# Optimization experiments

Hardware: AMD Instinct MI355X
Metric: run time of the kernel (lower is better)

Reference implementation:

```python
import jax, jax.numpy as jnp
import numpy as np
from jax import lax

B, C, L = 4, 256, 4
NA, NS, NAR = 3, 5, 4          # anchors, states, arrows
PRED_C = 4 + 1 + NS + NAR + 1  # 15 channels per anchor
HW = [(192, 320), (96, 160), (48, 80), (24, 40)]
EPS = 1e-5


def conv2d(x, w, b, pad):
    # x: (B,Cin,H,W), w: (Cout,Cin,kh,kw)
    y = lax.conv_general_dilated(x, w, (1, 1), ((pad, pad), (pad, pad)),
                                 dimension_numbers=('NCHW', 'OIHW', 'NCHW'))
    return y + b[None, :, None, None]


def bn(x, g, beta, m, v):
    # BatchNorm2d in inference mode with running stats
    scale = (g / jnp.sqrt(v + EPS))[None, :, None, None]
    return (x - m[None, :, None, None]) * scale + beta[None, :, None, None]


def setup_inputs() -> dict:
    key = jax.random.key(0)
    d = {}
    for i, (h, w) in enumerate(HW):
        d[f"feat{i}"] = jax.random.normal(jax.random.fold_in(key, i), (B, C, h, w), jnp.float32)
    ks = jax.random.split(jax.random.fold_in(key, 100), 8)
    d["adapt_w"] = jax.random.normal(ks[0], (L, C, C, 1, 1), jnp.float32) * 0.02
    d["adapt_b"] = jnp.zeros((L, C), jnp.float32)
    d["w1"] = jax.random.normal(ks[1], (L, C, C, 3, 3), jnp.float32) * 0.02
    d["b1"] = jnp.zeros((L, C), jnp.float32)
    d["g1"] = jnp.ones((L, C), jnp.float32)
    d["be1"] = jnp.zeros((L, C), jnp.float32)
    d["m1"] = jnp.zeros((L, C), jnp.float32)
    d["v1"] = jnp.ones((L, C), jnp.float32)
    d["w2"] = jax.random.normal(ks[2], (L, C, C, 3, 3), jnp.float32) * 0.02
    d["b2"] = jnp.zeros((L, C), jnp.float32)
    d["g2"] = jnp.ones((L, C), jnp.float32)
    d["be2"] = jnp.zeros((L, C), jnp.float32)
    d["m2"] = jnp.zeros((L, C), jnp.float32)
    d["v2"] = jnp.ones((L, C), jnp.float32)
    d["wp"] = jax.random.normal(ks[3], (L, NA * PRED_C, C, 1, 1), jnp.float32) * 0.02
    d["bp"] = jnp.zeros((L, NA * PRED_C), jnp.float32)
    return d


def reference(feat0, feat1, feat2, feat3, adapt_w, adapt_b,
              w1, b1, g1, be1, m1, v1,
              w2, b2, g2, be2, m2, v2, wp, bp):
    feats = [feat0, feat1, feat2, feat3]
    outs = []
    for i in range(L):
        x = conv2d(feats[i], adapt_w[i], adapt_b[i], 0)           # fpn_adapt 1x1
        x = jax.nn.relu(bn(conv2d(x, w1[i], b1[i], 1), g1[i], be1[i], m1[i], v1[i]))
        x = jax.nn.relu(bn(conv2d(x, w2[i], b2[i], 1), g2[i], be2[i], m2[i], v2[i]))
        p = conv2d(x, wp[i], bp[i], 0)                             # (B,45,H,W)
        Bb, _, H, W = p.shape
        p = p.reshape(Bb, NA, PRED_C, H, W)
        bbox = p[:, :, 0:4]
        obj = jax.nn.sigmoid(p[:, :, 4:5])
        state = p[:, :, 5:5 + NS]
        arrow = p[:, :, 5 + NS:5 + NS + NAR]
        dist = jax.nn.softplus(p[:, :, -1:]) + 1.0
        outs += [bbox, obj, state, arrow, dist]
    return tuple(outs)
```

## Files before the change

kernel.cpp:

```cpp
#include <hip/hip_runtime.h>
#include <math.h>

typedef __attribute__((ext_vector_type(8))) short bf16x8;
typedef __attribute__((ext_vector_type(4))) float f32x4;
typedef __attribute__((ext_vector_type(4))) unsigned short us4;

#define EPSV 1e-5f

__device__ inline unsigned short f2bf(float f){
  unsigned u = __float_as_uint(f);
  u += 0x7fff + ((u>>16)&1);
  return (unsigned short)(u>>16);
}

__device__ __forceinline__ void gload16(const unsigned short* g, char* l){
  __builtin_amdgcn_global_load_lds(
      (const __attribute__((address_space(1))) unsigned int*)g,
      (__attribute__((address_space(3))) unsigned int*)l, 16, 0, 0);
}

__global__ __launch_bounds__(256) void k_trans(const float* __restrict__ feat,
    unsigned short* __restrict__ ft, int H, int W, int Wp, int y_begin,
    int slot_base, int RBf)
{
  int t = threadIdx.x;
  int lane = t & 63, wv = t >> 6;
  int x = blockIdx.x*64 + lane;
  int y = y_begin + blockIdx.y;
  int b = blockIdx.z;
  int slot = slot_base + blockIdx.y;
  if (x >= W) return;
  const float* fb = feat + ((size_t)(b*256)*H + y)*W + x;
  unsigned short* dst = ft + (((size_t)b*RBf + slot)*Wp + x + 1)*256;
  #pragma unroll 4
  for (int i=0;i<16;i++){
    int c0 = wv*4 + i*16;
    float v0 = fb[(size_t)(c0+0)*H*W];
    float v1 = fb[(size_t)(c0+1)*H*W];
    float v2 = fb[(size_t)(c0+2)*H*W];
    float v3 = fb[(size_t)(c0+3)*H*W];
    us4 o = { f2bf(v0), f2bf(v1), f2bf(v2), f2bf(v3) };
    *(us4*)(dst + c0) = o;
  }
}

__global__ __launch_bounds__(256) void k_zrow(unsigned short* __restrict__ buf,
    long bStr, int Wp, int slot0, int nslots)
{
  long i = ((long)blockIdx.x*256 + threadIdx.x)*8;
  long per_b = (long)nslots*Wp*256;
  if (i >= 4*per_b) return;
  int b = (int)(i / per_b); long r = i % per_b;
  unsigned short* d = buf + (size_t)b*bStr + (size_t)slot0*Wp*256 + r;
  us4 z = {0,0,0,0};
  *(us4*)d = z; *(us4*)(d+4) = z;
}

__global__ __launch_bounds__(256) void k_zcol(unsigned short* __restrict__ buf,
    int Wp, int RB, int W)
{
  long i = ((long)blockIdx.x*256 + threadIdx.x)*8;
  long tot = (long)4*RB*2*256;
  if (i >= tot) return;
  long u = i/8; int q = (int)(u & 31); int side = (int)((u>>5)&1);
  long bs = u>>6; int slot = (int)(bs % RB); int b = (int)(bs / RB);
  unsigned short* d = buf + (((size_t)b*RB + slot)*Wp + (side? W+1 : 0))*256 + q*8;
  us4 z = {0,0,0,0};
  *(us4*)d = z; *(us4*)(d+4) = z;
}

__global__ __launch_bounds__(256) void k_repack_conv(const float* __restrict__ w,
    const float* __restrict__ g, const float* __restrict__ v,
    unsigned short* __restrict__ wf)
{
  int t = blockIdx.x*256 + threadIdx.x;
  if (t >= 4*256*256) return;
  int ci = t & 255, co = (t>>8) & 255, l = t>>16;
  float s = g[l*256+co] * rsqrtf(v[l*256+co] + EPSV);
  const float* wp = w + (size_t)t*9;
  int cb = co>>4, kc = ci>>5;
  int lane = ((ci>>3)&3)*16 + (co&15);
  int e = ci&7;
  size_t base = (((size_t)(l*16+cb)*8 + kc)*9)*512 + (size_t)lane*8 + e;
  #pragma unroll
  for (int tap=0;tap<9;tap++)
    wf[base + (size_t)tap*512] = f2bf(wp[tap]*s);
}

__global__ __launch_bounds__(256) void k_repack_conv_raw(const float* __restrict__ w,
    unsigned short* __restrict__ wf)
{
  int t = blockIdx.x*256 + threadIdx.x;
  if (t >= 4*256*256) return;
  int ci = t & 255, co = (t>>8) & 255, l = t>>16;
  const float* wp = w + (size_t)t*9;
  int cb = co>>4, kc = ci>>5;
  int lane = ((ci>>3)&3)*16 + (co&15);
  int e = ci&7;
  size_t base = (((size_t)(l*16+cb)*8 + kc)*9)*512 + (size_t)lane*8 + e;
  #pragma unroll
  for (int tap=0;tap<9;tap++)
    wf[base + (size_t)tap*512] = f2bf(wp[tap]);
}

__global__ __launch_bounds__(256) void k_repack_awB(const float* __restrict__ aw,
    unsigned short* __restrict__ out)
{
  int t = blockIdx.x*256 + threadIdx.x;
  if (t >= 4*16*8*64) return;
  int lane = t & 63, kc = (t>>6)&7, cit = (t>>9)&15, l = t>>13;
  int ci = cit*16 + (lane&15);
  int m0 = kc*32 + ((lane>>4))*8;
  unsigned short tmp[8];
  #pragma unroll
  for (int e=0;e<8;e++)
    tmp[e] = f2bf(aw[ ((size_t)(l*256 + m0 + e))*256 + ci ]);
  unsigned short* d = out + (size_t)t*8;
  *(us4*)d = *(us4*)tmp; *(us4*)(d+4) = *(us4*)(tmp+4);
}

__global__ __launch_bounds__(256) void k_fold(
    const unsigned short* __restrict__ w1raw,
    const unsigned short* __restrict__ bawB,
    const float* __restrict__ g, const float* __restrict__ v,
    unsigned short* __restrict__ wf)
{
  int blk = blockIdx.x;
  int cich = blk & 3;
  int tap  = (blk>>2) % 9;
  int l    = blk / 36;
  int tid = threadIdx.x, lane = tid&63, w = tid>>6;
  int l15 = lane&15, g4 = lane>>4;
  f32x4 acc[4][4];
  #pragma unroll
  for (int i=0;i<4;i++)
    #pragma unroll
    for (int j=0;j<4;j++) acc[i][j] = (f32x4){0.f,0.f,0.f,0.f};

  #pragma unroll 1
  for (int kc=0; kc<8; ++kc){
    bf16x8 A[4], B[4];
    #pragma unroll
    for (int cf=0;cf<4;cf++)
      A[cf] = *(const bf16x8*)(w1raw +
        ((((size_t)(l*16 + w*4+cf)*8 + kc)*9 + tap)*512) + (size_t)lane*8);
    #pragma unroll
    for (int pf=0;pf<4;pf++)
      B[pf] = *(const bf16x8*)(bawB +
        (((size_t)(l*16 + cich*4+pf)*8 + kc)*512) + (size_t)lane*8);
    #pragma unroll
    for (int cf=0;cf<4;cf++)
      #pragma unroll
      for (int pf=0;pf<4;pf++)
        acc[cf][pf] = __builtin_amdgcn_mfma_f32_16x16x32_bf16(A[cf], B[pf], acc[cf][pf], 0,0,0);
  }
  #pragma unroll
  for (int cf=0;cf<4;cf++){
    #pragma unroll
    for (int pf=0;pf<4;pf++){
      int ci = cich*64 + pf*16 + l15;
      #pragma unroll
      for (int r=0;r<4;r++){
        int co = w*64 + cf*16 + g4*4 + r;
        float s = g[l*256+co] * rsqrtf(v[l*256+co] + EPSV);
        float val = acc[cf][pf][r] * s;
        int cb = co>>4, kci = ci>>5;
        int dlane = ((ci>>3)&3)*16 + (co&15);
        int e = ci&7;
        wf[ ((((size_t)(l*16+cb)*8 + kci)*9 + tap)*512) + (size_t)dlane*8 + e ] = f2bf(val);
      }
    }
  }
}

__global__ __launch_bounds__(192) void k_repack_pred(const float* __restrict__ w,
    unsigned short* __restrict__ wf)
{
  int t = blockIdx.x*192 + threadIdx.x;
  if (t >= 4*48*32) return;
  int o = t & 31, co = (t>>5)%48, l = t/1536;
  int ci0 = o*8, f = co>>4, kc = o>>2, lane = (o&3)*16 + (co&15);
  unsigned short* dst = wf + ((((size_t)l*8 + kc)*3 + f)*64 + lane)*8;
  #pragma unroll
  for (int e=0;e<8;e++){
    float val = (co<45) ? w[((size_t)(l*45+co)*256 + ci0 + e)] : 0.f;
    dst[e] = f2bf(val);
  }
}

__global__ __launch_bounds__(256) void k_bias(const float* __restrict__ b,
    const float* __restrict__ g, const float* __restrict__ be,
    const float* __restrict__ m, const float* __restrict__ v,
    float* __restrict__ out)
{
  int t = blockIdx.x*256 + threadIdx.x;
  if (t >= 1024) return;
  float s = g[t]*rsqrtf(v[t]+EPSV);
  out[t] = (b[t]-m[t])*s + be[t];
}

__global__ __launch_bounds__(256) void k_bias1f(
    const float* __restrict__ w1, const float* __restrict__ ab,
    const float* __restrict__ b1, const float* __restrict__ g1,
    const float* __restrict__ be1, const float* __restrict__ m1,
    const float* __restrict__ v1, float* __restrict__ bcase)
{
  int t = blockIdx.x*256 + threadIdx.x;
  if (t >= 1024) return;
  int co = t & 255, l = t >> 8;
  float tt[9] = {0,0,0,0,0,0,0,0,0};
  const float* wp  = w1 + ((size_t)(l*256+co)*256)*9;
  const float* abp = ab + l*256;
  for (int m=0;m<256;m++){
    float a = abp[m];
    const float* w9 = wp + (size_t)m*9;
    #pragma unroll
    for (int tap=0;tap<9;tap++) tt[tap] += w9[tap]*a;
  }
  float s = g1[t]*rsqrtf(v1[t]+EPSV);
  float base = be1[t] + s*(b1[t]-m1[t]);
  for (int yc=0;yc<3;yc++)
    for (int xc=0;xc<3;xc++){
      float sum = 0.f;
      #pragma unroll
      for (int tap=0;tap<9;tap++){
        int ky = tap/3, kx = tap%3;
        bool oob = (yc==0&&ky==0)||(yc==2&&ky==2)||(xc==0&&kx==0)||(xc==2&&kx==2);
        if (!oob) sum += tt[tap];
      }
      bcase[ ((size_t)(l*9) + yc*3+xc)*256 + co ] = base + s*sum;
    }
}

template<int TAPS, bool RELU, bool PRED, bool FOLD>
__global__ __launch_bounds__(256,2) void k_conv6(
    const unsigned short* __restrict__ in, const unsigned short* __restrict__ wf,
    const float* __restrict__ bias, unsigned short* __restrict__ outb,
    int W, int Wp, int y_begin, int y_end, int in_row0, int RBin,
    int out_row0, int RBout,
    const unsigned short* __restrict__ wfP, const float* __restrict__ bp,
    float* __restrict__ outP, int H)
{
  constexpr bool T9    = (TAPS==9);
  constexpr int ROWS   = T9 ? 4 : 2;
  constexpr int PXS    = T9 ? 72 : 64;
  constexpr int RSTR   = PXS*64;
  constexpr int BUFB   = ROWS*RSTR;
  constexpr int NCHK   = BUFB/1024;
  constexpr int NFULL  = NCHK/4;
  constexpr int NTAIL  = NCHK - NFULL*4;
  constexpr int CPW    = NFULL + (NTAIL?1:0);
  constexpr int PERROW = PXS*4;
  constexpr int LDSB   = PRED ? (2*BUFB > 65536 ? 2*BUFB : 65536) : 2*BUFB;
  __shared__ __align__(1024) char lds[LDSB];

  int tid = threadIdx.x, lane = tid&63, w = tid>>6;
  int l15 = lane&15, g4 = lane>>4;
  int x0 = blockIdx.x*64;
  int y0 = y_begin + 2*blockIdx.y;
  int b  = blockIdx.z;

  size_t rowEl = (size_t)Wp*256;
  const unsigned short* gb =
      in + ((size_t)b*RBin + (y0-1-in_row0))*rowEl + (size_t)x0*256;

  int Poff[CPW], Coff[CPW];
  #pragma unroll
  for (int i=0;i<CPW;i++){
    int c = (i<NFULL) ? (4*i + w) : (4*NFULL + w);
    int s = c*64 + lane;
    int r = s / PERROW;
    int rem = s - r*PERROW;
    int px = rem>>2, sq = rem&3;
    int slot = sq ^ (px&3) ^ ((px>>2)&3);
    Poff[i] = r*(int)rowEl + px*256 + slot*8;
    Coff[i] = c*1024;
  }

  int vb[12];
  #pragma unroll
  for (int kx=0;kx<3;kx++)
    #pragma unroll
    for (int pf=0;pf<4;pf++){
      int px = pf*16 + l15 + kx;
      vb[kx*4+pf] = px*64 + ((g4 ^ (px&3) ^ ((px>>2)&3))<<4);
    }

  const unsigned short* wA = wf + (size_t)(w*4)*(8*TAPS*512) + (size_t)lane*8;

  f32x4 acc0[4][4], acc1[4][4];
  #pragma unroll
  for (int i=0;i<4;i++)
    #pragma unroll
    for (int j=0;j<4;j++){
      acc0[i][j] = (f32x4){0.f,0.f,0.f,0.f};
      acc1[i][j] = (f32x4){0.f,0.f,0.f,0.f};
    }

  const unsigned short* gbk = gb;
  auto stage = [&](int jb){
    #pragma unroll
    for (int i=0;i<NFULL;i++) gload16(gbk + Poff[i], (char*)&lds[0] + jb + Coff[i]);
    if constexpr (NTAIL > 0){
      if (w < NTAIL) gload16(gbk + Poff[NFULL], (char*)&lds[0] + jb + Coff[NFULL]);
    }
    gbk += 32;
  };

#define LOADB(KY, KX, BV) { \
  _Pragma("unroll") \
  for (int pf=0;pf<4;pf++) BV[pf] = *(const bf16x8*)(base + (KY)*RSTR + vb[(KX)*4+pf]); }

#define LOADA(G, AV) { \
  _Pragma("unroll") \
  for (int cf=0;cf<4;cf++) AV[cf] = *(const bf16x8*)(wk + (size_t)cf*(8*TAPS*512) + (G)*512); }

#define MM(AC, AV, BV) { \
  _Pragma("unroll") for (int cf=0;cf<4;cf++) \
  _Pragma("unroll") for (int pf=0;pf<4;pf++) \
    AC[cf][pf] = __builtin_amdgcn_mfma_f32_16x16x32_bf16(AV[cf], BV[pf], AC[cf][pf], 0,0,0); }

  auto compute = [&](int kc, const char* base){
    const unsigned short* wk = wA + (size_t)kc*(TAPS*512);
    bf16x8 A[4], B0[4], B1[4];
    #pragma unroll
    for (int kx=0;kx<3;kx++){
      LOADB(0,kx,B0) LOADB(1,kx,B1)
      LOADA(0*3+kx,A) MM(acc0,A,B0) MM(acc1,A,B1)
      LOADB(2,kx,B0)
      LOADA(1*3+kx,A) MM(acc0,A,B1) MM(acc1,A,B0)
      LOADB(3,kx,B1)
      LOADA(2*3+kx,A) MM(acc0,A,B0) MM(acc1,A,B1)
    }
  };

  stage(0);
  __syncthreads();
  #pragma unroll 1
  for (int kt=0; kt<4; ++kt){
    stage(BUFB);
    compute(2*kt, (const char*)&lds[0]);
    __syncthreads();
    if (kt < 3) stage(0);
    compute(2*kt+1, (const char*)&lds[0] + BUFB);
    __syncthreads();
  }
#undef LOADB
#undef LOADA
#undef MM

  if constexpr (!PRED){
    bool ok1 = (y0 + 1) < y_end;
    int oslot = y0 - out_row0;
    unsigned short* ob = outb + ((size_t)b*RBout + oslot)*rowEl + 256;
    int yc0 = 1, yc1 = 1;
    if constexpr (FOLD){
      yc0 = (y0==0)?0:((y0==H-1)?2:1);
      yc1 = (y0+1==0)?0:((y0+1==H-1)?2:1);
    }
    #pragma unroll
    for (int cf=0; cf<4; ++cf){
      int co0 = w*64 + cf*16 + g4*4;
      f32x4 bbI = *(const f32x4*)(bias + (FOLD ? 4*256 : 0) + co0);
      #pragma unroll
      for (int pf=0; pf<4; ++pf){
        int x = x0 + pf*16 + l15;
        if (x < W){
          f32x4 b0 = bbI, b1v = bbI;
          if constexpr (FOLD){
            int xc = (x==0)?0:((x==W-1)?2:1);
            b0  = *(const f32x4*)(bias + (yc0*3+xc)*256 + co0);
            b1v = *(const f32x4*)(bias + (yc1*3+xc)*256 + co0);
          }
          float v0 = acc0[cf][pf][0]+b0[0], v1 = acc0[cf][pf][1]+b0[1];
          float v2 = acc0[cf][pf][2]+b0[2], v3 = acc0[cf][pf][3]+b0[3];
          if (RELU){ v0=fmaxf(v0,0.f); v1=fmaxf(v1,0.f); v2=fmaxf(v2,0.f); v3=fmaxf(v3,0.f); }
          us4 o = { f2bf(v0), f2bf(v1), f2bf(v2), f2bf(v3) };
          *(us4*)(ob + (size_t)x*256 + co0) = o;
          if (ok1){
            float u0 = acc1[cf][pf][0]+b1v[0], u1 = acc1[cf][pf][1]+b1v[1];
            float u2 = acc1[cf][pf][2]+b1v[2], u3 = acc1[cf][pf][3]+b1v[3];
            if (RELU){ u0=fmaxf(u0,0.f); u1=fmaxf(u1,0.f); u2=fmaxf(u2,0.f); u3=fmaxf(u3,0.f); }
            us4 o1 = { f2bf(u0), f2bf(u1), f2bf(u2), f2bf(u3) };
            *(us4*)(ob + rowEl + (size_t)x*256 + co0) = o1;
          }
        }
      }
    }
  } else {
    __syncthreads();
    unsigned short* xs = (unsigned short*)&lds[0];
    #pragma unroll
    for (int cf=0; cf<4; ++cf){
      int co0 = w*64 + cf*16 + g4*4;
      f32x4 bb = *(const f32x4*)(bias + co0);
      int c16 = co0 >> 3;
      int sub = (g4 & 1) * 8;
      #pragma unroll
      for (int pf=0; pf<4; ++pf){
        int px = pf*16 + l15;
        int slot = c16 ^ (px & 31);
        float v0 = fmaxf(acc0[cf][pf][0]+bb[0],0.f), v1 = fmaxf(acc0[cf][pf][1]+bb[1],0.f);
        float v2 = fmaxf(acc0[cf][pf][2]+bb[2],0.f), v3 = fmaxf(acc0[cf][pf][3]+bb[3],0.f);
        us4 o0 = { f2bf(v0), f2bf(v1), f2bf(v2), f2bf(v3) };
        *(us4*)((char*)xs + ((px*32 + slot)<<4) + sub) = o0;
        float u0 = fmaxf(acc1[cf][pf][0]+bb[0],0.f), u1 = fmaxf(acc1[cf][pf][1]+bb[1],0.f);
        float u2 = fmaxf(acc1[cf][pf][2]+bb[2],0.f), u3 = fmaxf(acc1[cf][pf][3]+bb[3],0.f);
        us4 o1 = { f2bf(u0), f2bf(u1), f2bf(u2), f2bf(u3) };
        *(us4*)((char*)xs + 32768 + ((px*32 + slot)<<4) + sub) = o1;
      }
    }
    __syncthreads();

    int rw2 = w & 1, pxg = w >> 1;
    f32x4 ap[3][2];
    #pragma unroll
    for (int f=0;f<3;f++){ ap[f][0] = (f32x4){0,0,0,0}; ap[f][1] = (f32x4){0,0,0,0}; }
    #pragma unroll
    for (int kc=0;kc<8;kc++){
      bf16x8 Bf[2];
      #pragma unroll
      for (int t2=0;t2<2;t2++){
        int px = (pxg*2+t2)*16 + l15;
        int slot = (kc*4 + g4) ^ (px & 31);
        Bf[t2] = *(const bf16x8*)((char*)xs + rw2*32768 + ((px*32 + slot)<<4));
      }
      #pragma unroll
      for (int f=0;f<3;f++){
        bf16x8 Af = *(const bf16x8*)(wfP + (((size_t)kc*3 + f)*64 + lane)*8);
        ap[f][0] = __builtin_amdgcn_mfma_f32_16x16x32_bf16(Af, Bf[0], ap[f][0], 0,0,0);
        ap[f][1] = __builtin_amdgcn_mfma_f32_16x16x32_bf16(Af, Bf[1], ap[f][1], 0,0,0);
      }
    }
    int y = y0 + rw2;
    if (y < y_end){
      size_t S = (size_t)H*W;
      #pragma unroll
      for (int f=0;f<3;f++){
        #pragma unroll
        for (int t2=0;t2<2;t2++){
          int px = x0 + (pxg*2+t2)*16 + l15;
          if (px < W){
            #pragma unroll
            for (int r=0;r<4;r++){
              int co = f*16 + g4*4 + r;
              if (co < 45){
                float val = ap[f][t2][r] + bp[co];
                int a_idx = co/15, c = co%15;
                int cum,c0,n;
                if (c<4)       {cum=0;c0=0;n=4;}
                else if (c==4) {cum=4;c0=4;n=1;}
                else if (c<10) {cum=5;c0=5;n=5;}
                else if (c<14) {cum=10;c0=10;n=4;}
                else           {cum=14;c0=14;n=1;}
                if (c==4) val = 1.f/(1.f+expf(-val));
                else if (c==14) val = (val>20.f? val : log1pf(expf(val))) + 1.f;
                size_t chan = ((size_t)(12*cum) + (size_t)((b*3+a_idx)*n + (c-c0)))*S;
                outP[chan + (size_t)y*W + px] = val;
              }
            }
          }
        }
      }
    }
  }
}

extern "C" void kernel_launch(void* const* d_in, const int* in_sizes, int n_in,
                              void* d_out, int out_size, void* d_ws, size_t ws_size,
                              hipStream_t stream)
{
  static const int Hs[4] = {192,96,48,24};
  static const int Wd[4] = {320,160,80,40};
  const float* feat[4] = {(const float*)d_in[0],(const float*)d_in[1],
                          (const float*)d_in[2],(const float*)d_in[3]};
  const float* adapt_w = (const float*)d_in[4];
  const float* adapt_b = (const float*)d_in[5];
  const float* w1 = (const float*)d_in[6];  const float* b1 = (const float*)d_in[7];
  const float* g1 = (const float*)d_in[8];  const float* be1= (const float*)d_in[9];
  const float* m1 = (const float*)d_in[10]; const float* v1 = (const float*)d_in[11];
  const float* w2 = (const float*)d_in[12]; const float* b2 = (const float*)d_in[13];
  const float* g2 = (const float*)d_in[14]; const float* be2= (const float*)d_in[15];
  const float* m2 = (const float*)d_in[16]; const float* v2 = (const float*)d_in[17];
  const float* wp = (const float*)d_in[18]; const float* bp = (const float*)d_in[19];
  float* out = (float*)d_out;

  char* base = (char*)d_ws;
  size_t off = 0;
  auto alloc = [&](size_t bytes)->char*{
    char* p = base + off; off = (off + bytes + 255) & ~(size_t)255; return p; };

  const size_t WF3_L = (size_t)16*8*9*512;
  const size_t WAB_L = (size_t)16*8*512;
  const size_t WFP_L = (size_t)8*3*512;
  unsigned short* wf1raw = (unsigned short*)alloc(4*WF3_L*2);
  unsigned short* bawB   = (unsigned short*)alloc(4*WAB_L*2);
  unsigned short* wf1f   = (unsigned short*)alloc(4*WF3_L*2);
  unsigned short* wf2    = (unsigned short*)alloc(4*WF3_L*2);
  unsigned short* wfP    = (unsigned short*)alloc(4*WFP_L*2);
  float* bcase1 = (float*)alloc(4*9*256*4);
  float* biasc2 = (float*)alloc(1024*4);
  char*  bufbase = base + off;
  size_t rem = (ws_size > off + 65536) ? (ws_size - off - 65536) : 0;

  k_repack_conv_raw<<<dim3(1024), dim3(256), 0, stream>>>(w1, wf1raw);
  k_repack_awB     <<<dim3(128),  dim3(256), 0, stream>>>(adapt_w, bawB);
  k_repack_conv    <<<dim3(1024), dim3(256), 0, stream>>>(w2, g2, v2, wf2);
  k_repack_pred    <<<dim3(32),   dim3(192), 0, stream>>>(wp, wfP);
  k_bias1f<<<dim3(4), dim3(256), 0, stream>>>(w1, adapt_b, b1, g1, be1, m1, v1, bcase1);
  k_bias  <<<dim3(4), dim3(256), 0, stream>>>(b2, g2, be2, m2, v2, biasc2);
  k_fold  <<<dim3(144), dim3(256), 0, stream>>>(wf1raw, bawB, g1, v1, wf1f);

  size_t out_off = 0;
  for (int l=0;l<4;l++){
    int H = Hs[l], W = Wd[l], Wp = W + 2;
    size_t S = (size_t)H*W;
    size_t rowEl = (size_t)Wp*256;
    long slotsAvail = (long)(rem / (rowEl*2));
    long Rl = (slotsAvail - 60) / 8;
    int R = (int)(Rl < 2 ? 2 : (Rl > H ? (long)H : Rl));
    int RBf = R + 4, RB1 = R + 2;
    unsigned short* featT = (unsigned short*)bufbase;
    unsigned short* buf1  = featT + ((size_t)4*RBf + 8)*rowEl;
    int nPxT = (W + 63) / 64;
    long zcGrid0 = ((long)4*RBf*2*256 + 2047)/2048;
    long zcGrid1 = ((long)4*RB1*2*256 + 2047)/2048;
    k_zcol<<<dim3((unsigned)zcGrid0), dim3(256), 0, stream>>>(featT, Wp, RBf, W);
    k_zcol<<<dim3((unsigned)zcGrid1), dim3(256), 0, stream>>>(buf1, Wp, RB1, W);

    for (int r0 = 0; r0 < H; r0 += R){
      int r1 = (r0 + R < H) ? (r0 + R) : H;
      int Rc = r1 - r0;
      int ya0 = (r0-2 < 0) ? 0 : r0-2;
      int ya1 = (r1+2 > H) ? H : r1+2;
      int yb0 = (r0-1 < 0) ? 0 : r0-1;
      int yb1 = (r1+1 > H) ? H : r1+1;

      if (r0 == 0){
        long zg = ((long)4*2*Wp*256 + 2047)/2048;
        k_zrow<<<dim3((unsigned)zg), dim3(256), 0, stream>>>(featT, (long)RBf*Wp*256, Wp, 0, 2);
        long zg1 = ((long)4*1*Wp*256 + 2047)/2048;
        k_zrow<<<dim3((unsigned)zg1), dim3(256), 0, stream>>>(buf1, (long)RB1*Wp*256, Wp, 0, 1);
      }
      if (r1 == H){
        long zg = ((long)4*2*Wp*256 + 2047)/2048;
        k_zrow<<<dim3((unsigned)zg), dim3(256), 0, stream>>>(featT, (long)RBf*Wp*256, Wp, Rc+2, 2);
        long zg1 = ((long)4*1*Wp*256 + 2047)/2048;
        k_zrow<<<dim3((unsigned)zg1), dim3(256), 0, stream>>>(buf1, (long)RB1*Wp*256, Wp, Rc+1, 1);
      }

      k_trans<<<dim3(nPxT, ya1-ya0, 4), dim3(256), 0, stream>>>(
          feat[l], featT, H, W, Wp, ya0, ya0-(r0-2), RBf);

      k_conv6<9,true,false,true><<<dim3(nPxT, (yb1-yb0+1)/2, 4), dim3(256), 0, stream>>>(
          featT, wf1f + (size_t)l*WF3_L, bcase1 + (size_t)l*9*256, buf1,
          W, Wp, yb0, yb1, r0-2, RBf, r0-1, RB1,
          nullptr, nullptr, nullptr, H);

      k_conv6<9,true,true,false><<<dim3(nPxT, (Rc+1)/2, 4), dim3(256), 0, stream>>>(
          buf1, wf2 + (size_t)l*WF3_L, biasc2 + l*256, nullptr,
          W, Wp, r0, r1, r0-1, RB1, 0, 0,
          wfP + (size_t)l*WFP_L, bp + l*45, out + out_off, H);
    }
    out_off += (size_t)4*45*S;
  }
}
```

Measured before the change: 1.538 ms.

## Batch all pyramid levels into single fused transpose and conv launches

Adds a fused path used when the workspace can hold every level's full padded buffers at once. Halo zeroing, the feature transpose, conv1 and conv2+prediction each run as one launch across all four levels, with a per-block level lookup through cumulative block counts. This removes the per-level, per-row-chunk launch loop and the tail underfill of small levels. The cost is a larger workspace footprint and some extra index arithmetic per block.

```diff
diff --git a/kernel.cpp b/kernel.cpp
--- a/kernel.cpp
+++ b/kernel.cpp
@@ -17,6 +17,303 @@
   __builtin_amdgcn_global_load_lds(
       (const __attribute__((address_space(1))) unsigned int*)g,
       (__attribute__((address_space(3))) unsigned int*)l, 16, 0, 0);
+}
+
+struct TrP {
+  int cum[5];
+  int W[4], Wp[4], H[4], nPx[4];
+  unsigned long long ftOff[4];
+};
+struct CvP {
+  int cum[5];
+  int W[4], Wp[4], H[4], nPx[4], nRows[4];
+  unsigned long long inOff[4], outOff[4], outPOff[4];
+};
+#define NZJOB 32
+struct ZTab {
+  unsigned long long off[NZJOB];
+  unsigned long long cum[NZJOB+1];
+  int rowLen[NZJOB];
+  int rowStride[NZJOB];
+};
+
+__global__ __launch_bounds__(256) void k_zeroB(unsigned short* ws, ZTab T){
+  long long idx = (long long)blockIdx.x*256 + threadIdx.x;
+  if (idx >= (long long)T.cum[NZJOB]) return;
+  int j = 0;
+  #pragma unroll
+  for (int k=1;k<NZJOB;k++) j += (idx >= (long long)T.cum[k]);
+  long long r = idx - (long long)T.cum[j];
+  int spr = T.rowLen[j] >> 3;
+  int row = (int)(r / spr), c = (int)(r % spr);
+  unsigned short* d = ws + T.off[j] + (size_t)row*T.rowStride[j] + (size_t)c*8;
+  us4 z = {0,0,0,0};
+  *(us4*)d = z; *(us4*)(d+4) = z;
+}
+
+__global__ __launch_bounds__(256) void k_transF(const float* __restrict__ f0,
+    const float* __restrict__ f1, const float* __restrict__ f2,
+    const float* __restrict__ f3, unsigned short* __restrict__ ws, TrP P)
+{
+  int bx = blockIdx.x;
+  int l = (bx>=P.cum[1]) + (bx>=P.cum[2]) + (bx>=P.cum[3]);
+  int r = bx - P.cum[l];
+  int nPx = P.nPx[l];
+  int pxt = r % nPx; r /= nPx;
+  int H = P.H[l];
+  int y = r % H; int b = r / H;
+  int W = P.W[l], Wp = P.Wp[l];
+  const float* feat = (l==0)?f0:(l==1)?f1:(l==2)?f2:f3;
+  int t = threadIdx.x, lane = t & 63, wv = t >> 6;
+  int x = pxt*64 + lane;
+  if (x >= W) return;
+  const float* fb = feat + ((size_t)(b*256)*H + y)*W + x;
+  unsigned short* dst = ws + P.ftOff[l] + (((size_t)b*(H+4) + (y+2))*Wp + x + 1)*256;
+  #pragma unroll 4
+  for (int i=0;i<16;i++){
+    int c0 = wv*4 + i*16;
+    float v0 = fb[(size_t)(c0+0)*H*W];
+    float v1 = fb[(size_t)(c0+1)*H*W];
+    float v2 = fb[(size_t)(c0+2)*H*W];
+    float v3 = fb[(size_t)(c0+3)*H*W];
+    us4 o = { f2bf(v0), f2bf(v1), f2bf(v2), f2bf(v3) };
+    *(us4*)(dst + c0) = o;
+  }
+}
+
+template<bool PRED>
+__global__ __launch_bounds__(256,2) void k_convF(
+    unsigned short* __restrict__ ws, CvP P,
+    const unsigned short* __restrict__ wfB, const float* __restrict__ biasB,
+    const unsigned short* __restrict__ wfPB, const float* __restrict__ bpB,
+    float* __restrict__ outB)
+{
+  constexpr int ROWS   = 4;
+  constexpr int PXS    = 72;
+  constexpr int RSTR   = PXS*64;
+  constexpr int BUFB   = ROWS*RSTR;
+  constexpr int NCHK   = BUFB/1024;
+  constexpr int NFULL  = NCHK/4;
+  constexpr int NTAIL  = NCHK - NFULL*4;
+  constexpr int CPW    = NFULL + 1;
+  constexpr int PERROW = PXS*4;
+  constexpr int LDSB   = PRED ? 65536 : 2*BUFB;
+  __shared__ __align__(1024) char lds[LDSB];
+
+  int bx = blockIdx.x;
+  int l = (bx>=P.cum[1]) + (bx>=P.cum[2]) + (bx>=P.cum[3]);
+  int r = bx - P.cum[l];
+  int nPx = P.nPx[l];
+  int pxt = r % nPx; r /= nPx;
+  int nR = P.nRows[l];
+  int row = r % nR; int b = r / nR;
+  int W = P.W[l], Wp = P.Wp[l], H = P.H[l];
+  int RBin = H + (PRED ? 2 : 4);
+  int y0 = 2*row;
+
+  const unsigned short* in = ws + P.inOff[l];
+  const unsigned short* wf = wfB + (size_t)l*((size_t)16*8*9*512);
+  const float* bias = biasB + (size_t)l*(PRED ? 256 : 9*256);
+
+  int tid = threadIdx.x, lane = tid&63, w = tid>>6;
+  int l15 = lane&15, g4 = lane>>4;
+  int x0 = pxt*64;
+
+  size_t rowEl = (size_t)Wp*256;
+  const unsigned short* gb =
+      in + ((size_t)b*RBin + (size_t)(PRED ? y0 : y0+1))*rowEl + (size_t)x0*256;
+
+  int Poff[CPW], Coff[CPW];
+  #pragma unroll
+  for (int i=0;i<CPW;i++){
+    int c = (i<NFULL) ? (4*i + w) : (4*NFULL + w);
+    int s = c*64 + lane;
+    int rr = s / PERROW;
+    int rem = s - rr*PERROW;
+    int px = rem>>2, sq = rem&3;
+    int slot = sq ^ (px&3) ^ ((px>>2)&3);
+    Poff[i] = rr*(int)rowEl + px*256 + slot*8;
+    Coff[i] = c*1024;
+  }
+
+  int vb[12];
+  #pragma unroll
+  for (int kx=0;kx<3;kx++)
+    #pragma unroll
+    for (int pf=0;pf<4;pf++){
+      int px = pf*16 + l15 + kx;
+      vb[kx*4+pf] = px*64 + ((g4 ^ (px&3) ^ ((px>>2)&3))<<4);
+    }
+
+  const unsigned short* wA = wf + (size_t)(w*4)*(8*9*512) + (size_t)lane*8;
+
+  f32x4 acc0[4][4], acc1[4][4];
+  #pragma unroll
+  for (int i=0;i<4;i++)
+    #pragma unroll
+    for (int j=0;j<4;j++){
+      acc0[i][j] = (f32x4){0.f,0.f,0.f,0.f};
+      acc1[i][j] = (f32x4){0.f,0.f,0.f,0.f};
+    }
+
+  const unsigned short* gbk = gb;
+  auto stage = [&](int jb){
+    #pragma unroll
+    for (int i=0;i<NFULL;i++) gload16(gbk + Poff[i], (char*)&lds[0] + jb + Coff[i]);
+    if (w < NTAIL) gload16(gbk + Poff[NFULL], (char*)&lds[0] + jb + Coff[NFULL]);
+    gbk += 32;
+  };
+
+#define LOADB(KY, KX, BV) { \
+  _Pragma("unroll") \
+  for (int pf=0;pf<4;pf++) BV[pf] = *(const bf16x8*)(base + (KY)*RSTR + vb[(KX)*4+pf]); }
+
+#define LOADA(G, AV) { \
+  _Pragma("unroll") \
+  for (int cf=0;cf<4;cf++) AV[cf] = *(const bf16x8*)(wk + (size_t)cf*(8*9*512) + (G)*512); }
+
+#define MM(AC, AV, BV) { \
+  _Pragma("unroll") for (int cf=0;cf<4;cf++) \
+  _Pragma("unroll") for (int pf=0;pf<4;pf++) \
+    AC[cf][pf] = __builtin_amdgcn_mfma_f32_16x16x32_bf16(AV[cf], BV[pf], AC[cf][pf], 0,0,0); }
+
+  auto compute = [&](int kc, const char* base){
+    const unsigned short* wk = wA + (size_t)kc*(9*512);
+    bf16x8 A[4], B0[4], B1[4];
+    #pragma unroll
+    for (int kx=0;kx<3;kx++){
+      LOADB(0,kx,B0) LOADB(1,kx,B1)
+      LOADA(0*3+kx,A) MM(acc0,A,B0) MM(acc1,A,B1)
+      LOADB(2,kx,B0)
+      LOADA(1*3+kx,A) MM(acc0,A,B1) MM(acc1,A,B0)
+      LOADB(3,kx,B1)
+      LOADA(2*3+kx,A) MM(acc0,A,B0) MM(acc1,A,B1)
+    }
+  };
+
+  stage(0);
+  __syncthreads();
+  #pragma unroll 1
+  for (int kt=0; kt<4; ++kt){
+    stage(BUFB);
+    compute(2*kt, (const char*)&lds[0]);
+    __syncthreads();
+    if (kt < 3) stage(0);
+    compute(2*kt+1, (const char*)&lds[0] + BUFB);
+    __syncthreads();
+  }
+#undef LOADB
+#undef LOADA
+#undef MM
+
+  if constexpr (!PRED){
+    bool ok1 = (y0 + 1) < H;
+    unsigned short* ob = ws + P.outOff[l] + ((size_t)b*(H+2) + (y0+1))*rowEl + 256;
+    int yc0 = (y0==0)?0:((y0==H-1)?2:1);
+    int yc1 = (y0+1==0)?0:((y0+1==H-1)?2:1);
+    #pragma unroll
+    for (int cf=0; cf<4; ++cf){
+      int co0 = w*64 + cf*16 + g4*4;
+      #pragma unroll
+      for (int pf=0; pf<4; ++pf){
+        int x = x0 + pf*16 + l15;
+        if (x < W){
+          int xc = (x==0)?0:((x==W-1)?2:1);
+          f32x4 b0  = *(const f32x4*)(bias + (yc0*3+xc)*256 + co0);
+          f32x4 b1v = *(const f32x4*)(bias + (yc1*3+xc)*256 + co0);
+          float v0 = fmaxf(acc0[cf][pf][0]+b0[0],0.f), v1 = fmaxf(acc0[cf][pf][1]+b0[1],0.f);
+          float v2 = fmaxf(acc0[cf][pf][2]+b0[2],0.f), v3 = fmaxf(acc0[cf][pf][3]+b0[3],0.f);
+          us4 o = { f2bf(v0), f2bf(v1), f2bf(v2), f2bf(v3) };
+          *(us4*)(ob + (size_t)x*256 + co0) = o;
+          if (ok1){
+            float u0 = fmaxf(acc1[cf][pf][0]+b1v[0],0.f), u1 = fmaxf(acc1[cf][pf][1]+b1v[1],0.f);
+            float u2 = fmaxf(acc1[cf][pf][2]+b1v[2],0.f), u3 = fmaxf(acc1[cf][pf][3]+b1v[3],0.f);
+            us4 o1 = { f2bf(u0), f2bf(u1), f2bf(u2), f2bf(u3) };
+            *(us4*)(ob + rowEl + (size_t)x*256 + co0) = o1;
+          }
+        }
+      }
+    }
+  } else {
+    __syncthreads();
+    unsigned short* xs = (unsigned short*)&lds[0];
+    #pragma unroll
+    for (int cf=0; cf<4; ++cf){
+      int co0 = w*64 + cf*16 + g4*4;
+      f32x4 bb = *(const f32x4*)(bias + co0);
+      int c16 = co0 >> 3;
+      int sub = (g4 & 1) * 8;
+      #pragma unroll
+      for (int pf=0; pf<4; ++pf){
+        int px = pf*16 + l15;
+        int slot = c16 ^ (px & 31);
+        float v0 = fmaxf(acc0[cf][pf][0]+bb[0],0.f), v1 = fmaxf(acc0[cf][pf][1]+bb[1],0.f);
+        float v2 = fmaxf(acc0[cf][pf][2]+bb[2],0.f), v3 = fmaxf(acc0[cf][pf][3]+bb[3],0.f);
+        us4 o0 = { f2bf(v0), f2bf(v1), f2bf(v2), f2bf(v3) };
+        *(us4*)((char*)xs + ((px*32 + slot)<<4) + sub) = o0;
+        float u0 = fmaxf(acc1[cf][pf][0]+bb[0],0.f), u1 = fmaxf(acc1[cf][pf][1]+bb[1],0.f);
+        float u2 = fmaxf(acc1[cf][pf][2]+bb[2],0.f), u3 = fmaxf(acc1[cf][pf][3]+bb[3],0.f);
+        us4 o1 = { f2bf(u0), f2bf(u1), f2bf(u2), f2bf(u3) };
+        *(us4*)((char*)xs + 32768 + ((px*32 + slot)<<4) + sub) = o1;
+      }
+    }
+    __syncthreads();
+
+    const unsigned short* wfP = wfPB + (size_t)l*((size_t)8*3*512);
+    const float* bp = bpB + l*45;
+    float* outP = outB + P.outPOff[l];
+    int rw2 = w & 1, pxg = w >> 1;
+    f32x4 ap[3][2];
+    #pragma unroll
+    for (int f=0;f<3;f++){ ap[f][0] = (f32x4){0,0,0,0}; ap[f][1] = (f32x4){0,0,0,0}; }
+    #pragma unroll
+    for (int kc=0;kc<8;kc++){
+      bf16x8 Bf[2];
+      #pragma unroll
+      for (int t2=0;t2<2;t2++){
+        int px = (pxg*2+t2)*16 + l15;
+        int slot = (kc*4 + g4) ^ (px & 31);
+        Bf[t2] = *(const bf16x8*)((char*)xs + rw2*32768 + ((px*32 + slot)<<4));
+      }
+      #pragma unroll
+      for (int f=0;f<3;f++){
+        bf16x8 Af = *(const bf16x8*)(wfP + (((size_t)kc*3 + f)*64 + lane)*8);
+        ap[f][0] = __builtin_amdgcn_mfma_f32_16x16x32_bf16(Af, Bf[0], ap[f][0], 0,0,0);
+        ap[f][1] = __builtin_amdgcn_mfma_f32_16x16x32_bf16(Af, Bf[1], ap[f][1], 0,0,0);
+      }
+    }
+    int y = y0 + rw2;
+    if (y < H){
+      size_t S = (size_t)H*W;
+      #pragma unroll
+      for (int f=0;f<3;f++){
+        #pragma unroll
+        for (int t2=0;t2<2;t2++){
+          int px = x0 + (pxg*2+t2)*16 + l15;
+          if (px < W){
+            #pragma unroll
+            for (int rr=0;rr<4;rr++){
+              int co = f*16 + g4*4 + rr;
+              if (co < 45){
+                float val = ap[f][t2][rr] + bp[co];
+                int a_idx = co/15, c = co%15;
+                int cum,c0,n;
+                if (c<4)       {cum=0;c0=0;n=4;}
+                else if (c==4) {cum=4;c0=4;n=1;}
+                else if (c<10) {cum=5;c0=5;n=5;}
+                else if (c<14) {cum=10;c0=10;n=4;}
+                else           {cum=14;c0=14;n=1;}
+                if (c==4) val = 1.f/(1.f+expf(-val));
+                else if (c==14) val = (val>20.f? val : log1pf(expf(val))) + 1.f;
+                size_t chan = ((size_t)(12*cum) + (size_t)((b*3+a_idx)*n + (c-c0)))*S;
+                outP[chan + (size_t)y*W + px] = val;
+              }
+            }
+          }
+        }
+      }
+    }
+  }
 }
 
 __global__ __launch_bounds__(256) void k_trans(const float* __restrict__ feat,
@@ -241,17 +538,16 @@
     const unsigned short* __restrict__ wfP, const float* __restrict__ bp,
     float* __restrict__ outP, int H)
 {
-  constexpr bool T9    = (TAPS==9);
-  constexpr int ROWS   = T9 ? 4 : 2;
-  constexpr int PXS    = T9 ? 72 : 64;
+  constexpr int ROWS   = 4;
+  constexpr int PXS    = 72;
   constexpr int RSTR   = PXS*64;
   constexpr int BUFB   = ROWS*RSTR;
   constexpr int NCHK   = BUFB/1024;
   constexpr int NFULL  = NCHK/4;
   constexpr int NTAIL  = NCHK - NFULL*4;
-  constexpr int CPW    = NFULL + (NTAIL?1:0);
+  constexpr int CPW    = NFULL + 1;
   constexpr int PERROW = PXS*4;
-  constexpr int LDSB   = PRED ? (2*BUFB > 65536 ? 2*BUFB : 65536) : 2*BUFB;
+  constexpr int LDSB   = PRED ? 65536 : 2*BUFB;
   __shared__ __align__(1024) char lds[LDSB];
 
   int tid = threadIdx.x, lane = tid&63, w = tid>>6;
@@ -301,9 +597,7 @@
   auto stage = [&](int jb){
     #pragma unroll
     for (int i=0;i<NFULL;i++) gload16(gbk + Poff[i], (char*)&lds[0] + jb + Coff[i]);
-    if constexpr (NTAIL > 0){
-      if (w < NTAIL) gload16(gbk + Poff[NFULL], (char*)&lds[0] + jb + Coff[NFULL]);
-    }
+    if (w < NTAIL) gload16(gbk + Poff[NFULL], (char*)&lds[0] + jb + Coff[NFULL]);
     gbk += 32;
   };
 
@@ -511,6 +805,67 @@
   k_bias  <<<dim3(4), dim3(256), 0, stream>>>(b2, g2, be2, m2, v2, biasc2);
   k_fold  <<<dim3(144), dim3(256), 0, stream>>>(wf1raw, bawB, g1, v1, wf1f);
 
+  size_t ftOff[4], b1Off[4], cur = 0;
+  for (int l=0;l<4;l++){
+    int H = Hs[l], Wp = Wd[l]+2;
+    size_t rowEl = (size_t)Wp*256;
+    ftOff[l] = cur; cur += (size_t)4*(H+4)*rowEl;
+    b1Off[l] = cur; cur += (size_t)4*(H+2)*rowEl;
+  }
+  bool fused = (rem >= cur*2);
+
+  if (fused){
+    unsigned short* wsbuf = (unsigned short*)bufbase;
+
+    ZTab Z; unsigned long long zc = 0;
+    int j = 0;
+    for (int l=0;l<4;l++){
+      int H = Hs[l], W = Wd[l], Wp = W+2;
+      size_t rowEl = (size_t)Wp*256;
+      int RBf = H+4, RB1 = H+2;
+      Z.off[j]=ftOff[l];                    Z.rowLen[j]=(int)(2*rowEl); Z.rowStride[j]=(int)((size_t)RBf*rowEl); Z.cum[j]=zc; zc += (unsigned long long)4*(2*rowEl/8); j++;
+      Z.off[j]=ftOff[l]+(size_t)(H+2)*rowEl;Z.rowLen[j]=(int)(2*rowEl); Z.rowStride[j]=(int)((size_t)RBf*rowEl); Z.cum[j]=zc; zc += (unsigned long long)4*(2*rowEl/8); j++;
+      Z.off[j]=ftOff[l];                    Z.rowLen[j]=256; Z.rowStride[j]=(int)rowEl; Z.cum[j]=zc; zc += (unsigned long long)4*RBf*32; j++;
+      Z.off[j]=ftOff[l]+(size_t)(W+1)*256;  Z.rowLen[j]=256; Z.rowStride[j]=(int)rowEl; Z.cum[j]=zc; zc += (unsigned long long)4*RBf*32; j++;
+      Z.off[j]=b1Off[l];                    Z.rowLen[j]=(int)rowEl; Z.rowStride[j]=(int)((size_t)RB1*rowEl); Z.cum[j]=zc; zc += (unsigned long long)4*(rowEl/8); j++;
+      Z.off[j]=b1Off[l]+(size_t)(H+1)*rowEl;Z.rowLen[j]=(int)rowEl; Z.rowStride[j]=(int)((size_t)RB1*rowEl); Z.cum[j]=zc; zc += (unsigned long long)4*(rowEl/8); j++;
+      Z.off[j]=b1Off[l];                    Z.rowLen[j]=256; Z.rowStride[j]=(int)rowEl; Z.cum[j]=zc; zc += (unsigned long long)4*RB1*32; j++;
+      Z.off[j]=b1Off[l]+(size_t)(W+1)*256;  Z.rowLen[j]=256; Z.rowStride[j]=(int)rowEl; Z.cum[j]=zc; zc += (unsigned long long)4*RB1*32; j++;
+    }
+    Z.cum[NZJOB] = zc;
+    unsigned zgrid = (unsigned)((zc + 255) / 256);
+    k_zeroB<<<dim3(zgrid), dim3(256), 0, stream>>>(wsbuf, Z);
+
+    TrP T; T.cum[0] = 0;
+    for (int l=0;l<4;l++){
+      T.W[l]=Wd[l]; T.Wp[l]=Wd[l]+2; T.H[l]=Hs[l];
+      T.nPx[l]=(Wd[l]+63)/64; T.ftOff[l]=ftOff[l];
+      T.cum[l+1] = T.cum[l] + T.nPx[l]*Hs[l]*4;
+    }
+    k_transF<<<dim3((unsigned)T.cum[4]), dim3(256), 0, stream>>>(
+        feat[0], feat[1], feat[2], feat[3], wsbuf, T);
+
+    CvP C1, C2; C1.cum[0]=0; C2.cum[0]=0;
+    size_t out_off = 0;
+    for (int l=0;l<4;l++){
+      int H=Hs[l], W=Wd[l];
+      C1.W[l]=C2.W[l]=W; C1.Wp[l]=C2.Wp[l]=W+2; C1.H[l]=C2.H[l]=H;
+      C1.nPx[l]=C2.nPx[l]=(W+63)/64;
+      int nR=(H+1)/2;
+      C1.nRows[l]=C2.nRows[l]=nR;
+      C1.inOff[l]=ftOff[l];  C1.outOff[l]=b1Off[l]; C1.outPOff[l]=0;
+      C2.inOff[l]=b1Off[l];  C2.outOff[l]=0;        C2.outPOff[l]=out_off;
+      int cnt = C1.nPx[l]*nR*4;
+      C1.cum[l+1]=C1.cum[l]+cnt; C2.cum[l+1]=C2.cum[l]+cnt;
+      out_off += (size_t)4*45*H*W;
+    }
+    k_convF<false><<<dim3((unsigned)C1.cum[4]), dim3(256), 0, stream>>>(
+        wsbuf, C1, wf1f, bcase1, wfP, bp, out);
+    k_convF<true><<<dim3((unsigned)C2.cum[4]), dim3(256), 0, stream>>>(
+        wsbuf, C2, wf2, biasc2, wfP, bp, out);
+    return;
+  }
+
   size_t out_off = 0;
   for (int l=0;l<4;l++){
     int H = Hs[l], W = Wd[l], Wp = W + 2;
```

After: 1.261 ms. 18.0% less time.
